# Performance work log

Measured on AMD Instinct MI355X. Metric: run time of the kernel, lower is better.

The kernel has to match this reference:

```python
import jax, jax.numpy as jnp
import numpy as np

NUM_BINS = 256
BN_EPS = 1e-5


def setup_inputs() -> dict:
    key = jax.random.key(0)
    ks = jax.random.split(key, 16)
    B, C, H, W = 16, 64, 256, 256
    x = jax.random.uniform(ks[0], (B, C, H, W), dtype=jnp.float32) * 255.0
    return {
        "x": x,
        "conv1_w": jax.random.normal(ks[1], (C, C), dtype=jnp.float32) * 0.05,
        "conv1_b": jax.random.normal(ks[2], (C,), dtype=jnp.float32) * 0.05,
        "bn1_gamma": jax.random.uniform(ks[3], (C,), dtype=jnp.float32) + 0.5,
        "bn1_beta": jax.random.normal(ks[4], (C,), dtype=jnp.float32) * 0.05,
        "bn1_mean": jax.random.normal(ks[5], (C,), dtype=jnp.float32) * 0.05,
        "bn1_var": jax.random.uniform(ks[6], (C,), dtype=jnp.float32) + 0.5,
        "conv2_w": jax.random.normal(ks[7], (1, C), dtype=jnp.float32) * 0.05,
        "conv2_b": jax.random.normal(ks[8], (1,), dtype=jnp.float32) * 0.05,
        "bn2_gamma": jax.random.uniform(ks[9], (1,), dtype=jnp.float32) + 0.5,
        "bn2_beta": jax.random.normal(ks[10], (1,), dtype=jnp.float32) * 0.05,
        "bn2_mean": jax.random.normal(ks[11], (1,), dtype=jnp.float32) * 0.05,
        "bn2_var": jax.random.uniform(ks[12], (1,), dtype=jnp.float32) + 0.5,
    }


def _histc_argmax(x):
    # Replicates torch.histc(v, bins=NUM_BINS, min=0, max=255) per (b, c)
    # followed by argmax over bins. Out-of-range values are ignored by histc.
    B, C, H, W = x.shape
    flat = x.reshape(B * C, H * W)
    in_range = (flat >= 0.0) & (flat <= 255.0)
    # histc bin index: floor((v - min) * bins / (max - min)); v == max -> last bin
    idx = jnp.clip((flat * (NUM_BINS / 255.0)).astype(jnp.int32), 0, NUM_BINS - 1)
    rows = jnp.arange(B * C)[:, None]
    hist = jnp.zeros((B * C, NUM_BINS), dtype=jnp.float32).at[rows, idx].add(
        in_range.astype(jnp.float32)
    )
    return hist.argmax(axis=-1).reshape(B, C)  # [B, C] dominant bin indices


def _bn(a, gamma, beta, mean, var):
    inv = gamma * jax.lax.rsqrt(var + BN_EPS)
    return a * inv[None, :, None, None] + (beta - mean * inv)[None, :, None, None]


def reference(x, conv1_w, conv1_b, bn1_gamma, bn1_beta, bn1_mean, bn1_var,
              conv2_w, conv2_b, bn2_gamma, bn2_beta, bn2_mean, bn2_var):
    bin_size = 256 // NUM_BINS  # == 1 for default num_bins
    dominant = _histc_argmax(x)  # [B, C]
    # per-pixel bin index: torch's x.float() // bin_size then .long()
    pixel_bins = jnp.floor(x / bin_size).astype(jnp.int32)  # [B, C, H, W]
    att = (pixel_bins != dominant[:, :, None, None]).astype(x.dtype)
    # conv1 (1x1) -> bn1 -> relu
    a = jnp.einsum('bchw,oc->bohw', att, conv1_w) + conv1_b[None, :, None, None]
    a = jax.nn.relu(_bn(a, bn1_gamma, bn1_beta, bn1_mean, bn1_var))
    # conv2 (1x1, C->1) -> bn2 -> sigmoid
    a = jnp.einsum('bchw,oc->bohw', a, conv2_w) + conv2_b[None, :, None, None]
    a = jax.nn.sigmoid(_bn(a, bn2_gamma, bn2_beta, bn2_mean, bn2_var))
    return x * a
```

## Files before the change

### kernel.cpp

```cpp
#include <hip/hip_runtime.h>
#include <stdint.h>

#define CCH 64
#define HWPIX 65536
#define NBINS 256


__global__ __launch_bounds__(64) void precomp_kernel(
    const float* __restrict__ w1, const float* __restrict__ b1,
    const float* __restrict__ g1, const float* __restrict__ be1,
    const float* __restrict__ m1, const float* __restrict__ v1,
    const float* __restrict__ w2, const float* __restrict__ b2,
    const float* __restrict__ g2, const float* __restrict__ be2,
    const float* __restrict__ m2, const float* __restrict__ v2,
    float* __restrict__ ws)
{
    int o = threadIdx.x;
    float inv1 = g1[o] * rsqrtf(v1[o] + 1e-5f);
    float S = 0.f;
    for (int c = 0; c < CCH; ++c) S += w1[o * CCH + c];
    float beta1p = be1[o] - m1[o] * inv1;
    float base_pre = (S + b1[o]) * inv1 + beta1p;
    for (int c = 0; c < CCH; ++c) ws[1024 + o * CCH + c] = w1[o * CCH + c] * inv1;
    ws[5120 + o] = base_pre;
    float w2o = w2[o];
    ws[5184 + o] = w2o;
    float t = fmaxf(base_pre, 0.f) * w2o;
    #pragma unroll
    for (int off = 32; off > 0; off >>= 1) t += __shfl_down(t, off, 64);
    if (o == 0) {
        float inv2 = g2[0] * rsqrtf(v2[0] + 1e-5f);
        float beta2p = be2[0] - m2[0] * inv2;
        float z = (t + b2[0]) * inv2 + beta2p;
        ws[5248] = inv2;
        ws[5249] = beta2p;
        ws[5250] = b2[0];
        ws[5251] = 1.f / (1.f + expf(-z));
    }
}

__global__ __launch_bounds__(256) void hist_kernel(
    const float* __restrict__ x, int* __restrict__ dom)
{
    __shared__ unsigned h[4][NBINS];
    __shared__ unsigned long long red[NBINS];
    int tid = threadIdx.x;
    const float4* xp = (const float4*)(x + (size_t)blockIdx.x * HWPIX);

    for (int i = tid; i < 4 * NBINS; i += 256) ((unsigned*)h)[i] = 0;
    __syncthreads();

    unsigned* hmine = h[tid >> 6];
    const float scale = 256.0f / 255.0f;
    #pragma unroll 4
    for (int t = 0; t < HWPIX / 4 / 256; ++t) {
        float4 v = xp[t * 256 + tid];
        float vv[4] = {v.x, v.y, v.z, v.w};
        #pragma unroll
        for (int j = 0; j < 4; ++j) {
            float f = vv[j];
            if (f >= 0.f && f <= 255.f) {
                int bi = (int)(f * scale);
                bi = bi > NBINS - 1 ? NBINS - 1 : bi;
                atomicAdd(&hmine[bi], 1u);
            }
        }
    }
    __syncthreads();

    unsigned cnt = h[0][tid] + h[1][tid] + h[2][tid] + h[3][tid];
    red[tid] = ((unsigned long long)cnt << 32) | (unsigned)(NBINS - 1 - tid);
    __syncthreads();
    #pragma unroll
    for (int s = 128; s > 0; s >>= 1) {
        if (tid < s) {
            unsigned long long a = red[tid], b = red[tid + s];
            red[tid] = a > b ? a : b;
        }
        __syncthreads();
    }
    if (tid == 0) dom[blockIdx.x] = (NBINS - 1) - (int)(red[0] & 0xffffffffu);
}

__global__ __launch_bounds__(256) void main_kernel(
    const float* __restrict__ x, const float* __restrict__ ws,
    const int* __restrict__ dom, float* __restrict__ out)
{
    __shared__ float WcolT[CCH * CCH];
    __shared__ float bp_s[CCH];
    __shared__ float w2_s[CCH];
    __shared__ int   dom_s[CCH];
    __shared__ float sc[4];

    int tid = threadIdx.x;
    int b = blockIdx.x >> 8;
    int hw = ((blockIdx.x & 255) << 8) | tid;

    for (int i = tid; i < CCH * CCH; i += 256) WcolT[i] = ws[1024 + i];
    if (tid < CCH) {
        bp_s[tid]  = ws[5120 + tid];
        w2_s[tid]  = ws[5184 + tid];
        dom_s[tid] = dom[b * CCH + tid];
    }
    if (tid < 4) sc[tid] = ws[5248 + tid];
    __syncthreads();

    const float* xb = x + ((size_t)b << 22);
    float vx[CCH];
    #pragma unroll
    for (int c = 0; c < CCH; ++c) vx[c] = xb[((size_t)c << 16) + hw];

    unsigned long long m = 0ull;
    #pragma unroll
    for (int c = 0; c < CCH; ++c)
        m |= (unsigned long long)((int)floorf(vx[c]) == dom_s[c]) << c;

    float s;
    if (m == 0ull) {
        s = sc[3];
    } else {
        float t = 0.f;
        for (int o = 0; o < CCH; ++o) {
            float acc = bp_s[o];
            unsigned long long mm = m;
            const float* row = &WcolT[o << 6];
            while (mm) {
                int c = __builtin_ctzll(mm);
                mm &= mm - 1;
                acc -= row[c];
            }
            t += fmaxf(acc, 0.f) * w2_s[o];
        }
        float z = (t + sc[2]) * sc[0] + sc[1];
        s = 1.f / (1.f + expf(-z));
    }

    float* ob = out + ((size_t)b << 22);
    #pragma unroll
    for (int c = 0; c < CCH; ++c) ob[((size_t)c << 16) + hw] = vx[c] * s;
}

extern "C" void kernel_launch(void* const* d_in, const int* in_sizes, int n_in,
                              void* d_out, int out_size, void* d_ws, size_t ws_size,
                              hipStream_t stream) {
    const float* x   = (const float*)d_in[0];
    const float* w1  = (const float*)d_in[1];
    const float* b1  = (const float*)d_in[2];
    const float* g1  = (const float*)d_in[3];
    const float* be1 = (const float*)d_in[4];
    const float* m1  = (const float*)d_in[5];
    const float* v1  = (const float*)d_in[6];
    const float* w2  = (const float*)d_in[7];
    const float* b2  = (const float*)d_in[8];
    const float* g2  = (const float*)d_in[9];
    const float* be2 = (const float*)d_in[10];
    const float* m2  = (const float*)d_in[11];
    const float* v2  = (const float*)d_in[12];

    float* ws  = (float*)d_ws;
    int*   dom = (int*)d_ws;
    float* outp = (float*)d_out;

    int B = in_sizes[0] / (CCH * HWPIX);

    precomp_kernel<<<1, 64, 0, stream>>>(w1, b1, g1, be1, m1, v1,
                                         w2, b2, g2, be2, m2, v2, ws);
    hist_kernel<<<B * CCH, 256, 0, stream>>>(x, dom);
    main_kernel<<<B * (HWPIX / 256), 256, 0, stream>>>(x, ws, dom, outp);
}
```

Baseline: 190.0 us.

## Stage pixel tiles in LDS, add single-hit sigmoid table, widen histogram privatization

The main kernel now loads a 64-channel by 128-pixel tile into shared memory with float4 loads and stores. The per-pixel mask and sigmoid are computed by half the threads and written to shared memory. The precompute kernel adds a per-channel table of sigmoid values for pixels whose mask has exactly one bit set, so the common single-match case skips the 64x64 inner loop. The histogram kernel uses 16 padded sub-histograms instead of 4 to reduce shared-atomic contention. In exchange, the main kernel uses more shared memory, which may lower occupancy, and only 128 of 256 threads do the mask work.

```diff
diff --git a/kernel.cpp b/kernel.cpp
--- a/kernel.cpp
+++ b/kernel.cpp
@@ -4,6 +4,7 @@
 #define CCH 64
 #define HWPIX 65536
 #define NBINS 256
+#define TPX 128
 
 
 __global__ __launch_bounds__(64) void precomp_kernel(
@@ -37,20 +38,31 @@
         ws[5250] = b2[0];
         ws[5251] = 1.f / (1.f + expf(-z));
     }
+    __syncthreads();
+    {
+        int c = o;
+        float t1 = 0.f;
+        for (int oo = 0; oo < CCH; ++oo) {
+            float acc = ws[5120 + oo] - ws[1024 + oo * CCH + c];
+            t1 += fmaxf(acc, 0.f) * ws[5184 + oo];
+        }
+        float z = (t1 + ws[5250]) * ws[5248] + ws[5249];
+        ws[5312 + c] = 1.f / (1.f + expf(-z));
+    }
 }
 
 __global__ __launch_bounds__(256) void hist_kernel(
     const float* __restrict__ x, int* __restrict__ dom)
 {
-    __shared__ unsigned h[4][NBINS];
+    __shared__ unsigned h[16][NBINS + 1];
     __shared__ unsigned long long red[NBINS];
     int tid = threadIdx.x;
     const float4* xp = (const float4*)(x + (size_t)blockIdx.x * HWPIX);
 
-    for (int i = tid; i < 4 * NBINS; i += 256) ((unsigned*)h)[i] = 0;
-    __syncthreads();
-
-    unsigned* hmine = h[tid >> 6];
+    for (int i = tid; i < 16 * (NBINS + 1); i += 256) ((unsigned*)h)[i] = 0;
+    __syncthreads();
+
+    unsigned* hmine = h[tid >> 4];
     const float scale = 256.0f / 255.0f;
     #pragma unroll 4
     for (int t = 0; t < HWPIX / 4 / 256; ++t) {
@@ -68,7 +80,9 @@
     }
     __syncthreads();
 
-    unsigned cnt = h[0][tid] + h[1][tid] + h[2][tid] + h[3][tid];
+    unsigned cnt = 0;
+    #pragma unroll
+    for (int k = 0; k < 16; ++k) cnt += h[k][tid];
     red[tid] = ((unsigned long long)cnt << 32) | (unsigned)(NBINS - 1 - tid);
     __syncthreads();
     #pragma unroll
@@ -86,58 +100,81 @@
     const float* __restrict__ x, const float* __restrict__ ws,
     const int* __restrict__ dom, float* __restrict__ out)
 {
-    __shared__ float WcolT[CCH * CCH];
+    __shared__ float tile[CCH * TPX];
+    __shared__ float Wrow[CCH * CCH];
+    __shared__ float ss[TPX];
     __shared__ float bp_s[CCH];
     __shared__ float w2_s[CCH];
+    __shared__ float s1_s[CCH];
     __shared__ int   dom_s[CCH];
     __shared__ float sc[4];
 
     int tid = threadIdx.x;
-    int b = blockIdx.x >> 8;
-    int hw = ((blockIdx.x & 255) << 8) | tid;
-
-    for (int i = tid; i < CCH * CCH; i += 256) WcolT[i] = ws[1024 + i];
+    int b = blockIdx.x >> 9;
+    int p0 = (blockIdx.x & 511) * TPX;
+
+    for (int i = tid; i < CCH * CCH; i += 256) Wrow[i] = ws[1024 + i];
     if (tid < CCH) {
         bp_s[tid]  = ws[5120 + tid];
         w2_s[tid]  = ws[5184 + tid];
+        s1_s[tid]  = ws[5312 + tid];
         dom_s[tid] = dom[b * CCH + tid];
     }
     if (tid < 4) sc[tid] = ws[5248 + tid];
-    __syncthreads();
-
-    const float* xb = x + ((size_t)b << 22);
-    float vx[CCH];
-    #pragma unroll
-    for (int c = 0; c < CCH; ++c) vx[c] = xb[((size_t)c << 16) + hw];
-
-    unsigned long long m = 0ull;
-    #pragma unroll
-    for (int c = 0; c < CCH; ++c)
-        m |= (unsigned long long)((int)floorf(vx[c]) == dom_s[c]) << c;
-
-    float s;
-    if (m == 0ull) {
-        s = sc[3];
-    } else {
-        float t = 0.f;
-        for (int o = 0; o < CCH; ++o) {
-            float acc = bp_s[o];
-            unsigned long long mm = m;
-            const float* row = &WcolT[o << 6];
-            while (mm) {
-                int c = __builtin_ctzll(mm);
-                mm &= mm - 1;
-                acc -= row[c];
+
+    const float4* xb4 = (const float4*)(x + ((size_t)b << 22));
+    float4* tile4 = (float4*)tile;
+    int p04 = p0 >> 2;
+    #pragma unroll
+    for (int k = 0; k < (CCH * TPX / 4) / 256; ++k) {
+        int id = k * 256 + tid;
+        int c = id >> 5, col = id & 31;
+        tile4[id] = xb4[((size_t)c << 14) + p04 + col];
+    }
+    __syncthreads();
+
+    if (tid < TPX) {
+        unsigned long long m = 0ull;
+        #pragma unroll
+        for (int c = 0; c < CCH; ++c) {
+            float v = tile[c * TPX + tid];
+            m |= (unsigned long long)((int)floorf(v) == dom_s[c]) << c;
+        }
+        float s;
+        if (m == 0ull) {
+            s = sc[3];
+        } else if ((m & (m - 1)) == 0ull) {
+            s = s1_s[__builtin_ctzll(m)];
+        } else {
+            float t = 0.f;
+            for (int o = 0; o < CCH; ++o) {
+                float acc = bp_s[o];
+                unsigned long long mm = m;
+                const float* row = &Wrow[o << 6];
+                while (mm) {
+                    int c = __builtin_ctzll(mm);
+                    mm &= mm - 1;
+                    acc -= row[c];
+                }
+                t += fmaxf(acc, 0.f) * w2_s[o];
             }
-            t += fmaxf(acc, 0.f) * w2_s[o];
-        }
-        float z = (t + sc[2]) * sc[0] + sc[1];
-        s = 1.f / (1.f + expf(-z));
-    }
-
-    float* ob = out + ((size_t)b << 22);
-    #pragma unroll
-    for (int c = 0; c < CCH; ++c) ob[((size_t)c << 16) + hw] = vx[c] * s;
+            float z = (t + sc[2]) * sc[0] + sc[1];
+            s = 1.f / (1.f + expf(-z));
+        }
+        ss[tid] = s;
+    }
+    __syncthreads();
+
+    float4* ob4 = (float4*)(out + ((size_t)b << 22));
+    #pragma unroll
+    for (int k = 0; k < (CCH * TPX / 4) / 256; ++k) {
+        int id = k * 256 + tid;
+        int c = id >> 5, col = id & 31;
+        float4 v = tile4[id];
+        const float4 sv = *(const float4*)&ss[col << 2];
+        v.x *= sv.x; v.y *= sv.y; v.z *= sv.z; v.w *= sv.w;
+        ob4[((size_t)c << 14) + p04 + col] = v;
+    }
 }
 
 extern "C" void kernel_launch(void* const* d_in, const int* in_sizes, int n_in,
@@ -166,5 +203,5 @@
     precomp_kernel<<<1, 64, 0, stream>>>(w1, b1, g1, be1, m1, v1,
                                          w2, b2, g2, be2, m2, v2, ws);
     hist_kernel<<<B * CCH, 256, 0, stream>>>(x, dom);
-    main_kernel<<<B * (HWPIX / 256), 256, 0, stream>>>(x, ws, dom, outp);
-}
+    main_kernel<<<B * (HWPIX / TPX), 256, 0, stream>>>(x, ws, dom, outp);
+}
```

Measured after the change: 262.3 us. 38.1% more time.
